# Performance work log

Hardware: AMD Instinct MI355X
Metric: run time of the kernel (lower is better)

The kernel has to match this reference:

```python
import jax, jax.numpy as jnp
import numpy as np

NEG = -1.0e9
LN_EPS = 1e-5

B, S, M = 16, 1024, 256
H, L = 8, 2
DK = M // H  # 32


def setup_inputs() -> dict:
    key = jax.random.key(0)
    ks = jax.random.split(key, 10)
    adj = jax.random.randint(ks[0], (B, S, S), 0, 2).astype(jnp.int32)
    inputs = jax.random.normal(ks[1], (B, S, M), dtype=jnp.float32)
    score_mask = jax.random.randint(ks[2], (B, 1, S, S), 0, 2).astype(bool)
    # learned params: per layer H head projections Linear(M, DK), one attn Linear(2*DK, 1), LayerNorm(M)
    sc = 1.0 / np.sqrt(M)
    proj_w = jax.random.uniform(ks[3], (L, H, M, DK), jnp.float32, -sc, sc)
    proj_b = jax.random.uniform(ks[4], (L, H, DK), jnp.float32, -sc, sc)
    sa = 1.0 / np.sqrt(2 * DK)
    attn_w = jax.random.uniform(ks[5], (L, 2 * DK), jnp.float32, -sa, sa)
    attn_b = jax.random.uniform(ks[6], (L,), jnp.float32, -sa, sa)
    ln_g = jnp.ones((L, M), jnp.float32)
    ln_b = jnp.zeros((L, M), jnp.float32)
    return {"adj": adj, "inputs": inputs, "score_mask": score_mask, "type": 0,
            "proj_w": proj_w, "proj_b": proj_b, "attn_w": attn_w, "attn_b": attn_b,
            "ln_g": ln_g, "ln_b": ln_b}


def _layer(x, adj_l, smask, pw, pb, aw, ab, g, b):
    # x: [B,S,M]; per-head projection -> [B,H,S,DK]
    P = jnp.einsum('bsm,hmd->bhsd', x, pw) + pb[None, :, None, :]
    a1, a2 = aw[:DK], aw[DK:]
    # additive attention decomposed: score[b,h,i,j] = leaky_relu(a1.P_i + a2.P_j + ab)
    s1 = jnp.einsum('bhsd,d->bhs', P, a1)
    s2 = jnp.einsum('bhsd,d->bhs', P, a2)
    score = s1[..., :, None] + s2[..., None, :] + ab
    score = jnp.where(score >= 0, score, 0.2 * score)  # leaky_relu(0.2)
    score = jnp.where(smask, NEG, score)               # score_mask[:,0] broadcast over heads
    if adj_l is not None:
        score = jnp.where(adj_l[:, None] == 0, NEG, score)
    attn = jax.nn.softmax(score, axis=-1)
    out = jnp.einsum('bhij,bhjd->bhid', attn, P)       # [B,H,S,DK]
    concat = out.transpose(0, 2, 1, 3).reshape(x.shape[0], x.shape[1], -1)
    r = x + concat
    mu = jnp.mean(r, axis=-1, keepdims=True)
    var = jnp.mean((r - mu) ** 2, axis=-1, keepdims=True)
    return (r - mu) * jax.lax.rsqrt(var + LN_EPS) * g + b


def reference(adj, inputs, score_mask, type, proj_w, proj_b, attn_w, attn_b, ln_g, ln_b):
    # eval mode: DropBlock and both dropouts are identity
    semantic = (type == 1)
    smask = score_mask[:, 0][:, None]  # [B,1,S,S]
    x = inputs
    for l in range(L):
        adj_l = None if (semantic and l > 0) else adj
        x = _layer(x, adj_l, smask, proj_w[l], proj_b[l], attn_w[l], attn_b[l], ln_g[l], ln_b[l])
    return x
```

## Files before the change

### kernel.cpp

```cpp
#include <hip/hip_runtime.h>
#include <hip/hip_bf16.h>
#include <hip/hip_fp16.h>
#include <math.h>

#define NB 16
#define NS 1024
#define NM 256
#define NH 8
#define NDK 32
#define NL 2

typedef __attribute__((ext_vector_type(4))) float f32x4;
typedef __attribute__((ext_vector_type(8))) short bf16x8;
typedef __attribute__((ext_vector_type(4))) short bf16x4u;
typedef __attribute__((ext_vector_type(8))) _Float16 f16x8;
typedef __attribute__((ext_vector_type(2))) _Float16 f16x2;

#if __has_builtin(__builtin_amdgcn_exp2f)
#define EXP2F(x) __builtin_amdgcn_exp2f(x)
#else
#define EXP2F(x) exp2f(x)
#endif

__device__ __forceinline__ unsigned short f2h(float f) {
  _Float16 h = (_Float16)f;
  return __builtin_bit_cast(unsigned short, h);
}

__device__ __forceinline__ unsigned int wword(unsigned int pw, unsigned int nw,
                                              f16x2 e1p2, f16x2 e1n2,
                                              unsigned int mk) {
  f16x2 hp = __builtin_bit_cast(f16x2, pw);
  f16x2 hn = __builtin_bit_cast(f16x2, nw);
  f16x2 w = __builtin_elementwise_max(hp * e1p2, hn * e1n2);
  return __builtin_bit_cast(unsigned int, w) & mk;
}

__global__ __launch_bounds__(256) void packbits_kernel(
    const int* __restrict__ src, unsigned int* __restrict__ dst, int inv,
    unsigned int* __restrict__ orc)
{
  int wid = blockIdx.x * 4 + (threadIdx.x >> 6);
  int lane = threadIdx.x & 63;
  size_t eb = (size_t)wid * 2048;
  const int4* a4 = (const int4*)(src + eb);
  int lg = lane >> 3;
  int sh = (lane & 7) * 4;
  unsigned int xo = inv ? 15u : 0u;
#pragma unroll
  for (int k = 0; k < 8; ++k) {
    int4 v = a4[k * 64 + lane];
    unsigned int nc = ((v.x != 0) ? 1u : 0u) | ((v.y != 0) ? 2u : 0u) |
                      ((v.z != 0) ? 4u : 0u) | ((v.w != 0) ? 8u : 0u);
    nc ^= xo;
    unsigned int vc = nc << sh;
    vc |= __shfl_xor(vc, 1, 64);
    vc |= __shfl_xor(vc, 2, 64);
    vc |= __shfl_xor(vc, 4, 64);
    if ((lane & 7) == 0) {
      size_t wi = (size_t)wid * 64 + k * 8 + lg;
      dst[wi] = vc;
      if (orc) orc[wi] |= vc;
    }
  }
}

__global__ __launch_bounds__(256) void wprep_kernel(
    const float* __restrict__ pw, unsigned short* __restrict__ Wt)
{
  __shared__ float lw[256][36];
  int lh = blockIdx.x;
  int t = threadIdx.x;
  const float* src = pw + (size_t)lh * NM * NDK;
#pragma unroll
  for (int q = 0; q < 8; ++q) {
    int e0 = q * 1024 + t * 4;
    int m = e0 >> 5, dc = e0 & 31;
    f32x4 v = *(const f32x4*)(src + e0);
    *(f32x4*)&lw[m][dc] = v;
  }
  __syncthreads();
  unsigned short* out = Wt + (size_t)lh * NDK * NM;
#pragma unroll
  for (int q = 0; q < 4; ++q) {
    int idx = q * 2048 + t * 8;
    int d = idx >> 8, m = idx & 255;
    unsigned short ov[8];
#pragma unroll
    for (int j = 0; j < 8; ++j) ov[j] = f2h(lw[m + j][d]);
    *(uint4*)(out + (size_t)d * NM + m) = *(uint4*)ov;
  }
}

__global__ __launch_bounds__(256) void proj_kernel(
    const float* __restrict__ x,
    const unsigned short* __restrict__ Wt,
    const float* __restrict__ pb,
    const float* __restrict__ aw,
    const float* __restrict__ abp,
    unsigned short* __restrict__ Pt,
    float* __restrict__ s1o,
    unsigned short* __restrict__ s2po,
    unsigned short* __restrict__ s2no)
{
  __shared__ unsigned short As[64][40];
  __shared__ unsigned short Bs[64][40];

  const float LOG2E = 1.4426950408889634f;
  int ct = blockIdx.x;
  int rt = blockIdx.y;
  int t = threadIdx.x;
  int w = t >> 6, lane = t & 63;
  int il = lane & 15, g4 = lane >> 4;
  int wi = w >> 1, wc = w & 1;

  f32x4 acc[2][2] = {};

  int arow = t >> 2, akoff = (t & 3) * 8;
  int brow = t >> 2, bkoff = (t & 3) * 8;

  for (int k0 = 0; k0 < NM; k0 += 32) {
    const float* xp = x + (size_t)(rt * 64 + arow) * NM + k0 + akoff;
    f32x4 v0 = *(const f32x4*)xp;
    f32x4 v1 = *(const f32x4*)(xp + 4);
    unsigned short av[8];
    av[0] = f2h(v0[0]); av[1] = f2h(v0[1]); av[2] = f2h(v0[2]); av[3] = f2h(v0[3]);
    av[4] = f2h(v1[0]); av[5] = f2h(v1[1]); av[6] = f2h(v1[2]); av[7] = f2h(v1[3]);
    *(uint4*)&As[arow][akoff] = *(uint4*)av;
    uint4 bv = *(const uint4*)(Wt + (size_t)(ct * 64 + brow) * NM + k0 + bkoff);
    *(uint4*)&Bs[brow][bkoff] = bv;
    __syncthreads();

    f16x8 af0 = *(f16x8*)&As[wi * 32 + il][g4 * 8];
    f16x8 af1 = *(f16x8*)&As[wi * 32 + 16 + il][g4 * 8];
    f16x8 bf0 = *(f16x8*)&Bs[wc * 32 + il][g4 * 8];
    f16x8 bf1 = *(f16x8*)&Bs[wc * 32 + 16 + il][g4 * 8];
    acc[0][0] = __builtin_amdgcn_mfma_f32_16x16x32_f16(af0, bf0, acc[0][0], 0, 0, 0);
    acc[0][1] = __builtin_amdgcn_mfma_f32_16x16x32_f16(af0, bf1, acc[0][1], 0, 0, 0);
    acc[1][0] = __builtin_amdgcn_mfma_f32_16x16x32_f16(af1, bf0, acc[1][0], 0, 0, 0);
    acc[1][1] = __builtin_amdgcn_mfma_f32_16x16x32_f16(af1, bf1, acc[1][1], 0, 0, 0);
    __syncthreads();
  }

  int head = ct * 2 + wc;
  float a1v[2] = {aw[il], aw[16 + il]};
  float a2v[2] = {aw[32 + il], aw[48 + il]};
  float ab = abp[0];

#pragma unroll
  for (int ih = 0; ih < 2; ++ih) {
    float s1p[4] = {0.f, 0.f, 0.f, 0.f};
    float s2p[4] = {0.f, 0.f, 0.f, 0.f};
    int r0 = rt * 64 + wi * 32 + ih * 16 + g4 * 4;
    int bb = r0 >> 10, ss = r0 & 1023;
#pragma unroll
    for (int dh = 0; dh < 2; ++dh) {
      int colhd = ct * 64 + wc * 32 + dh * 16 + il;
      int dd = colhd & 31;
      float bias = pb[colhd];
      f32x4 c = acc[ih][dh];
      unsigned short ov[4];
#pragma unroll
      for (int e = 0; e < 4; ++e) {
        float Pv = c[e] + bias;
        ov[e] = f2h(Pv);
        s1p[e] += Pv * a1v[dh];
        s2p[e] += Pv * a2v[dh];
      }
      size_t idx = ((size_t)(bb * NH + head) * NDK + dd) * NS + ss;
      *(bf16x4u*)(Pt + idx) = *(bf16x4u*)ov;
    }
#pragma unroll
    for (int e = 0; e < 4; ++e) {
#pragma unroll
      for (int off = 1; off <= 8; off <<= 1) {
        s1p[e] += __shfl_xor(s1p[e], off, 64);
        s2p[e] += __shfl_xor(s2p[e], off, 64);
      }
    }
    if (il == 0) {
      size_t sb = (size_t)(bb * NH + head) * NS + ss;
#pragma unroll
      for (int e = 0; e < 4; ++e) {
        s1o[sb + e] = s1p[e] * LOG2E;
        float s2L = (s2p[e] + ab) * LOG2E;
        s2L = fminf(fmaxf(s2L, -7.5f), 7.5f);
        s2po[sb + e] = f2h(EXP2F(s2L));
        s2no[sb + e] = f2h(EXP2F(0.2f * s2L));
      }
    }
  }
}

__global__ __launch_bounds__(512) void attn_kernel(
    const unsigned short* __restrict__ Pt,
    const float* __restrict__ s1a,
    const unsigned short* __restrict__ s2pa,
    const unsigned short* __restrict__ s2na,
    const unsigned int* __restrict__ pkc,
    const unsigned int* __restrict__ pks,
    const int* __restrict__ typep,
    int layer,
    float* __restrict__ co)
{
  __shared__ __align__(16) unsigned short ptl[32 * 512];
  __shared__ __align__(16) unsigned short e2pl[1024];
  __shared__ __align__(16) unsigned short e2nl[1024];
  __shared__ uint4 mtab[256];

  int orig = blockIdx.x;
  int lb = (orig & 7) * 64 + (orig >> 3);
  int iq = lb & 3, bh = lb >> 2;
  int b = bh >> 3, h = bh & 7;

  int t = threadIdx.x, w = t >> 6, lane = t & 63;
  int il = lane & 15, g4 = lane >> 4;
  int xorv = (il & 7) << 4;

  if (t < 256) {
    unsigned int m = t;
    uint4 e;
    e.x = ((m & 1u)   ? 0u : 0xFFFFu) | ((m & 2u)   ? 0u : 0xFFFF0000u);
    e.y = ((m & 4u)   ? 0u : 0xFFFFu) | ((m & 8u)   ? 0u : 0xFFFF0000u);
    e.z = ((m & 16u)  ? 0u : 0xFFFFu) | ((m & 32u)  ? 0u : 0xFFFF0000u);
    e.w = ((m & 64u)  ? 0u : 0xFFFFu) | ((m & 128u) ? 0u : 0xFFFF0000u);
    mtab[t] = e;
  }

  const unsigned char* pkb =
      (const unsigned char*)((typep[0] == 1 && layer > 0) ? pks : pkc);
  const unsigned short* ptg = Pt + (size_t)bh * NDK * NS;

  f16x8 ones;
#pragma unroll
  for (int e = 0; e < 8; ++e) ones[e] = (_Float16)1.0f;

  int rbase = iq * 256 + w * 32;
  f16x2 e1p2[2], e1n2[2];
  const unsigned char* mrow[2];
#pragma unroll
  for (int g = 0; g < 2; ++g) {
    float s1L = s1a[(size_t)bh * NS + rbase + g * 16 + il];
    s1L = fminf(fmaxf(s1L, -7.5f), 7.5f);
    _Float16 hp = (_Float16)EXP2F(s1L);
    _Float16 hn = (_Float16)EXP2F(0.2f * s1L);
    e1p2[g][0] = hp; e1p2[g][1] = hp;
    e1n2[g][0] = hn; e1n2[g][1] = hn;
    mrow[g] = pkb + (((size_t)(b * NS + rbase + g * 16 + il) * NS) >> 3);
  }

  f32x4 acc[2][2] = {};
  f32x4 accd[2] = {};

  for (int jh = 0; jh < 2; ++jh) {
    __syncthreads();
    {
      const char* srcb = (const char*)ptg;
#pragma unroll
      for (int q = 0; q < 4; ++q) {
        int pos = q * 8192 + t * 16;
        int r = pos >> 10;
        int incol = pos & 1023;
        uint4 v = *(const uint4*)(srcb + r * 2048 + jh * 1024 + incol);
        *(uint4*)((char*)ptl + r * 1024 + (incol ^ ((r & 7) << 4))) = v;
      }
      if (jh == 0) {
        if (t < 128)
          ((uint4*)e2pl)[t] = *(const uint4*)(s2pa + (size_t)bh * NS + t * 8);
        else if (t < 256)
          ((uint4*)e2nl)[t - 128] =
              *(const uint4*)(s2na + (size_t)bh * NS + (t - 128) * 8);
      }
    }
    __syncthreads();

    for (int jg = 0; jg < 512; jg += 128) {
      uint4 mk0 = *(const uint4*)(mrow[0] + ((jh * 512 + jg) >> 3));
      uint4 mk1 = *(const uint4*)(mrow[1] + ((jh * 512 + jg) >> 3));
#pragma unroll
      for (int s = 0; s < 4; ++s) {
        unsigned int mb0 = ((&mk0.x)[s] >> (g4 * 8)) & 0xFFu;
        unsigned int mb1 = ((&mk1.x)[s] >> (g4 * 8)) & 0xFFu;
        uint4 am0 = mtab[mb0];
        uint4 am1 = mtab[mb1];
        int jl = jg + s * 32 + g4 * 8;
        int coff = (jl * 2) ^ xorv;
        const char* prow = (const char*)ptl + il * 1024;
        f16x8 b0 = *(const f16x8*)(prow + coff);
        f16x8 b1 = *(const f16x8*)(prow + 16 * 1024 + coff);
        int jfull = jh * 512 + jl;
        uint4 p4 = *(const uint4*)&e2pl[jfull];
        uint4 n4 = *(const uint4*)&e2nl[jfull];
        uint4 w0, w1;
        w0.x = wword(p4.x, n4.x, e1p2[0], e1n2[0], am0.x);
        w0.y = wword(p4.y, n4.y, e1p2[0], e1n2[0], am0.y);
        w0.z = wword(p4.z, n4.z, e1p2[0], e1n2[0], am0.z);
        w0.w = wword(p4.w, n4.w, e1p2[0], e1n2[0], am0.w);
        w1.x = wword(p4.x, n4.x, e1p2[1], e1n2[1], am1.x);
        w1.y = wword(p4.y, n4.y, e1p2[1], e1n2[1], am1.y);
        w1.z = wword(p4.z, n4.z, e1p2[1], e1n2[1], am1.z);
        w1.w = wword(p4.w, n4.w, e1p2[1], e1n2[1], am1.w);
        f16x8 af0 = __builtin_bit_cast(f16x8, w0);
        f16x8 af1 = __builtin_bit_cast(f16x8, w1);
        acc[0][0] = __builtin_amdgcn_mfma_f32_16x16x32_f16(af0, b0, acc[0][0], 0, 0, 0);
        acc[0][1] = __builtin_amdgcn_mfma_f32_16x16x32_f16(af0, b1, acc[0][1], 0, 0, 0);
        accd[0]   = __builtin_amdgcn_mfma_f32_16x16x32_f16(af0, ones, accd[0], 0, 0, 0);
        acc[1][0] = __builtin_amdgcn_mfma_f32_16x16x32_f16(af1, b0, acc[1][0], 0, 0, 0);
        acc[1][1] = __builtin_amdgcn_mfma_f32_16x16x32_f16(af1, b1, acc[1][1], 0, 0, 0);
        accd[1]   = __builtin_amdgcn_mfma_f32_16x16x32_f16(af1, ones, accd[1], 0, 0, 0);
      }
    }
  }

#pragma unroll
  for (int g = 0; g < 2; ++g) {
    f32x4 rd;
#pragma unroll
    for (int e = 0; e < 4; ++e) rd[e] = __builtin_amdgcn_rcpf(accd[g][e]);
    float* cob = co + (size_t)(b * NS + rbase + g * 16 + g4 * 4) * NM + h * 32 + il;
#pragma unroll
    for (int e = 0; e < 4; ++e) {
      cob[(size_t)e * NM] = acc[g][0][e] * rd[e];
      cob[(size_t)e * NM + 16] = acc[g][1][e] * rd[e];
    }
  }
}

__global__ __launch_bounds__(256) void ln_kernel(
    const float* __restrict__ xin, const float* __restrict__ co,
    const float* __restrict__ lng, const float* __restrict__ lnb,
    float* __restrict__ xout)
{
  int row = blockIdx.x * 4 + (threadIdx.x >> 6);
  int lane = threadIdx.x & 63;
  size_t base = (size_t)row * NM + lane * 4;
  f32x4 cv = *(const f32x4*)(co + base);
  f32x4 xv = *(const f32x4*)(xin + base);
  f32x4 r;
#pragma unroll
  for (int e = 0; e < 4; ++e) r[e] = cv[e] + xv[e];
  float sm = r[0] + r[1] + r[2] + r[3];
  float sq = r[0] * r[0] + r[1] * r[1] + r[2] * r[2] + r[3] * r[3];
#pragma unroll
  for (int off = 32; off >= 1; off >>= 1) {
    sm += __shfl_xor(sm, off, 64);
    sq += __shfl_xor(sq, off, 64);
  }
  float mu = sm * (1.f / 256.f);
  float var = sq * (1.f / 256.f) - mu * mu;
  float inv = rsqrtf(var + 1e-5f);
  f32x4 gv = *(const f32x4*)(lng + lane * 4);
  f32x4 bv = *(const f32x4*)(lnb + lane * 4);
  f32x4 o;
#pragma unroll
  for (int e = 0; e < 4; ++e) o[e] = (r[e] - mu) * inv * gv[e] + bv[e];
  *(f32x4*)(xout + base) = o;
}

extern "C" void kernel_launch(void* const* d_in, const int* in_sizes, int n_in,
                              void* d_out, int out_size, void* d_ws, size_t ws_size,
                              hipStream_t stream)
{
  const int* adj = (const int*)d_in[0];
  const float* inputs = (const float*)d_in[1];
  const int* smask = (const int*)d_in[2];
  const int* typep = (const int*)d_in[3];
  const float* proj_w = (const float*)d_in[4];
  const float* proj_b = (const float*)d_in[5];
  const float* attn_w = (const float*)d_in[6];
  const float* attn_b = (const float*)d_in[7];
  const float* ln_g = (const float*)d_in[8];
  const float* ln_b = (const float*)d_in[9];
  float* out = (float*)d_out;

  char* ws = (char*)d_ws;
  unsigned int* pkc = (unsigned int*)(ws);
  unsigned int* pks = (unsigned int*)(ws + (2u << 20));
  unsigned short* Pt = (unsigned short*)(ws + (4u << 20));
  float* s1 = (float*)(ws + (12u << 20));
  unsigned short* s2p = (unsigned short*)(ws + (12u << 20) + (1u << 19));
  unsigned short* s2n = (unsigned short*)(ws + (13u << 20));
  float* x1 = (float*)(ws + (14u << 20));
  unsigned short* Wt = (unsigned short*)(ws + (30u << 20));
  float* co = out;

  packbits_kernel<<<2048, 256, 0, stream>>>(adj, pkc, 1, nullptr);
  packbits_kernel<<<2048, 256, 0, stream>>>(smask, pks, 0, pkc);
  wprep_kernel<<<16, 256, 0, stream>>>(proj_w, Wt);

  for (int l = 0; l < NL; ++l) {
    const float* xin = (l == 0) ? inputs : x1;
    float* xout = (l == NL - 1) ? out : x1;
    proj_kernel<<<dim3(4, 256), 256, 0, stream>>>(
        xin, Wt + (size_t)l * NH * NDK * NM, proj_b + (size_t)l * NH * NDK,
        attn_w + l * 64, attn_b + l, Pt, s1, s2p, s2n);
    attn_kernel<<<512, 512, 0, stream>>>(
        Pt, s1, s2p, s2n, pkc, pks, typep, l, co);
    ln_kernel<<<4096, 256, 0, stream>>>(xin, co, ln_g + l * NM, ln_b + l * NM, xout);
  }
}
```

Before: 128.0 us.

## Fuse mask packing with layer-0 projection and store attention output as fp16

Both mask-packing launches and the first-layer projection now run as one combined prelude kernel. The read-modify-write OR of the score mask into the adjacency bitmap is removed, so the attention kernel loads both bitmaps and ORs them on the fly. The attention output is written as fp16 to a workspace buffer instead of fp32, which halves that traffic, and the layernorm kernel reads it back in fp16. The trade-offs are extra mask loads in the attention inner loop and lower precision on the attention output before the residual add.

```diff
diff --git a/kernel.cpp b/kernel.cpp
--- a/kernel.cpp
+++ b/kernel.cpp
@@ -11,7 +11,6 @@
 #define NL 2
 
 typedef __attribute__((ext_vector_type(4))) float f32x4;
-typedef __attribute__((ext_vector_type(8))) short bf16x8;
 typedef __attribute__((ext_vector_type(4))) short bf16x4u;
 typedef __attribute__((ext_vector_type(8))) _Float16 f16x8;
 typedef __attribute__((ext_vector_type(2))) _Float16 f16x2;
@@ -25,6 +24,9 @@
 __device__ __forceinline__ unsigned short f2h(float f) {
   _Float16 h = (_Float16)f;
   return __builtin_bit_cast(unsigned short, h);
+}
+__device__ __forceinline__ float h2f(unsigned short u) {
+  return (float)__builtin_bit_cast(_Float16, u);
 }
 
 __device__ __forceinline__ unsigned int wword(unsigned int pw, unsigned int nw,
@@ -36,35 +38,6 @@
   return __builtin_bit_cast(unsigned int, w) & mk;
 }
 
-__global__ __launch_bounds__(256) void packbits_kernel(
-    const int* __restrict__ src, unsigned int* __restrict__ dst, int inv,
-    unsigned int* __restrict__ orc)
-{
-  int wid = blockIdx.x * 4 + (threadIdx.x >> 6);
-  int lane = threadIdx.x & 63;
-  size_t eb = (size_t)wid * 2048;
-  const int4* a4 = (const int4*)(src + eb);
-  int lg = lane >> 3;
-  int sh = (lane & 7) * 4;
-  unsigned int xo = inv ? 15u : 0u;
-#pragma unroll
-  for (int k = 0; k < 8; ++k) {
-    int4 v = a4[k * 64 + lane];
-    unsigned int nc = ((v.x != 0) ? 1u : 0u) | ((v.y != 0) ? 2u : 0u) |
-                      ((v.z != 0) ? 4u : 0u) | ((v.w != 0) ? 8u : 0u);
-    nc ^= xo;
-    unsigned int vc = nc << sh;
-    vc |= __shfl_xor(vc, 1, 64);
-    vc |= __shfl_xor(vc, 2, 64);
-    vc |= __shfl_xor(vc, 4, 64);
-    if ((lane & 7) == 0) {
-      size_t wi = (size_t)wid * 64 + k * 8 + lg;
-      dst[wi] = vc;
-      if (orc) orc[wi] |= vc;
-    }
-  }
-}
-
 __global__ __launch_bounds__(256) void wprep_kernel(
     const float* __restrict__ pw, unsigned short* __restrict__ Wt)
 {
@@ -92,32 +65,22 @@
   }
 }
 
-__global__ __launch_bounds__(256) void proj_kernel(
-    const float* __restrict__ x,
-    const unsigned short* __restrict__ Wt,
-    const float* __restrict__ pb,
-    const float* __restrict__ aw,
+__device__ __forceinline__ void proj_body(
+    int ct, int rt, int t,
+    const float* __restrict__ x, const unsigned short* __restrict__ Wt,
+    const float* __restrict__ pb, const float* __restrict__ aw,
     const float* __restrict__ abp,
-    unsigned short* __restrict__ Pt,
-    float* __restrict__ s1o,
-    unsigned short* __restrict__ s2po,
-    unsigned short* __restrict__ s2no)
-{
-  __shared__ unsigned short As[64][40];
-  __shared__ unsigned short Bs[64][40];
-
+    unsigned short* __restrict__ Pt, float* __restrict__ s1o,
+    unsigned short* __restrict__ s2po, unsigned short* __restrict__ s2no,
+    unsigned short (*As)[40], unsigned short (*Bs)[40])
+{
   const float LOG2E = 1.4426950408889634f;
-  int ct = blockIdx.x;
-  int rt = blockIdx.y;
-  int t = threadIdx.x;
   int w = t >> 6, lane = t & 63;
   int il = lane & 15, g4 = lane >> 4;
   int wi = w >> 1, wc = w & 1;
 
   f32x4 acc[2][2] = {};
-
   int arow = t >> 2, akoff = (t & 3) * 8;
-  int brow = t >> 2, bkoff = (t & 3) * 8;
 
   for (int k0 = 0; k0 < NM; k0 += 32) {
     const float* xp = x + (size_t)(rt * 64 + arow) * NM + k0 + akoff;
@@ -127,8 +90,8 @@
     av[0] = f2h(v0[0]); av[1] = f2h(v0[1]); av[2] = f2h(v0[2]); av[3] = f2h(v0[3]);
     av[4] = f2h(v1[0]); av[5] = f2h(v1[1]); av[6] = f2h(v1[2]); av[7] = f2h(v1[3]);
     *(uint4*)&As[arow][akoff] = *(uint4*)av;
-    uint4 bv = *(const uint4*)(Wt + (size_t)(ct * 64 + brow) * NM + k0 + bkoff);
-    *(uint4*)&Bs[brow][bkoff] = bv;
+    uint4 bv = *(const uint4*)(Wt + (size_t)(ct * 64 + arow) * NM + k0 + akoff);
+    *(uint4*)&Bs[arow][akoff] = bv;
     __syncthreads();
 
     f16x8 af0 = *(f16x8*)&As[wi * 32 + il][g4 * 8];
@@ -192,16 +155,72 @@
   }
 }
 
+__global__ __launch_bounds__(256) void prelude_kernel(
+    const int* __restrict__ adj, const int* __restrict__ smask,
+    unsigned int* __restrict__ pka, unsigned int* __restrict__ pks,
+    const float* __restrict__ x, const unsigned short* __restrict__ Wt0,
+    const float* __restrict__ pb0, const float* __restrict__ aw0,
+    const float* __restrict__ ab0,
+    unsigned short* __restrict__ Pt, float* __restrict__ s1o,
+    unsigned short* __restrict__ s2po, unsigned short* __restrict__ s2no)
+{
+  __shared__ unsigned short As[64][40];
+  __shared__ unsigned short Bs[64][40];
+
+  int bid = blockIdx.x;
+  int t = threadIdx.x;
+  if (bid < 4096) {
+    const int* src = (bid < 2048) ? adj : smask;
+    unsigned int* dst = (bid < 2048) ? pka : pks;
+    unsigned int xo = (bid < 2048) ? 15u : 0u;
+    int wid = (bid & 2047) * 4 + (t >> 6);
+    int lane = t & 63;
+    size_t eb = (size_t)wid * 2048;
+    const int4* a4 = (const int4*)(src + eb);
+    int lg = lane >> 3;
+    int sh = (lane & 7) * 4;
+#pragma unroll
+    for (int k = 0; k < 8; ++k) {
+      int4 v = a4[k * 64 + lane];
+      unsigned int nc = ((v.x != 0) ? 1u : 0u) | ((v.y != 0) ? 2u : 0u) |
+                        ((v.z != 0) ? 4u : 0u) | ((v.w != 0) ? 8u : 0u);
+      nc ^= xo;
+      unsigned int vc = nc << sh;
+      vc |= __shfl_xor(vc, 1, 64);
+      vc |= __shfl_xor(vc, 2, 64);
+      vc |= __shfl_xor(vc, 4, 64);
+      if ((lane & 7) == 0) dst[(size_t)wid * 64 + k * 8 + lg] = vc;
+    }
+  } else {
+    int pb2 = bid - 4096;
+    proj_body(pb2 & 3, pb2 >> 2, t, x, Wt0, pb0, aw0, ab0,
+              Pt, s1o, s2po, s2no, As, Bs);
+  }
+}
+
+__global__ __launch_bounds__(256) void proj_kernel(
+    const float* __restrict__ x, const unsigned short* __restrict__ Wt,
+    const float* __restrict__ pb, const float* __restrict__ aw,
+    const float* __restrict__ abp,
+    unsigned short* __restrict__ Pt, float* __restrict__ s1o,
+    unsigned short* __restrict__ s2po, unsigned short* __restrict__ s2no)
+{
+  __shared__ unsigned short As[64][40];
+  __shared__ unsigned short Bs[64][40];
+  proj_body(blockIdx.x, blockIdx.y, threadIdx.x, x, Wt, pb, aw, abp,
+            Pt, s1o, s2po, s2no, As, Bs);
+}
+
 __global__ __launch_bounds__(512) void attn_kernel(
     const unsigned short* __restrict__ Pt,
     const float* __restrict__ s1a,
     const unsigned short* __restrict__ s2pa,
     const unsigned short* __restrict__ s2na,
-    const unsigned int* __restrict__ pkc,
+    const unsigned int* __restrict__ pka,
     const unsigned int* __restrict__ pks,
     const int* __restrict__ typep,
     int layer,
-    float* __restrict__ co)
+    unsigned short* __restrict__ co)
 {
   __shared__ __align__(16) unsigned short ptl[32 * 512];
   __shared__ __align__(16) unsigned short e2pl[1024];
@@ -227,8 +246,9 @@
     mtab[t] = e;
   }
 
-  const unsigned char* pkb =
-      (const unsigned char*)((typep[0] == 1 && layer > 0) ? pks : pkc);
+  bool comb = !(typep[0] == 1 && layer > 0);
+  const unsigned char* pa = (const unsigned char*)(comb ? pka : pks);
+  const unsigned char* ps = (const unsigned char*)pks;
   const unsigned short* ptg = Pt + (size_t)bh * NDK * NS;
 
   f16x8 ones;
@@ -237,7 +257,7 @@
 
   int rbase = iq * 256 + w * 32;
   f16x2 e1p2[2], e1n2[2];
-  const unsigned char* mrow[2];
+  size_t mbyte[2];
 #pragma unroll
   for (int g = 0; g < 2; ++g) {
     float s1L = s1a[(size_t)bh * NS + rbase + g * 16 + il];
@@ -246,7 +266,7 @@
     _Float16 hn = (_Float16)EXP2F(0.2f * s1L);
     e1p2[g][0] = hp; e1p2[g][1] = hp;
     e1n2[g][0] = hn; e1n2[g][1] = hn;
-    mrow[g] = pkb + (((size_t)(b * NS + rbase + g * 16 + il) * NS) >> 3);
+    mbyte[g] = ((size_t)(b * NS + rbase + g * 16 + il) * NS) >> 3;
   }
 
   f32x4 acc[2][2] = {};
@@ -275,8 +295,16 @@
     __syncthreads();
 
     for (int jg = 0; jg < 512; jg += 128) {
-      uint4 mk0 = *(const uint4*)(mrow[0] + ((jh * 512 + jg) >> 3));
-      uint4 mk1 = *(const uint4*)(mrow[1] + ((jh * 512 + jg) >> 3));
+      size_t off = (size_t)((jh * 512 + jg) >> 3);
+      uint4 ka0 = *(const uint4*)(pa + mbyte[0] + off);
+      uint4 ks0 = *(const uint4*)(ps + mbyte[0] + off);
+      uint4 ka1 = *(const uint4*)(pa + mbyte[1] + off);
+      uint4 ks1 = *(const uint4*)(ps + mbyte[1] + off);
+      uint4 mk0, mk1;
+      mk0.x = ka0.x | ks0.x; mk0.y = ka0.y | ks0.y;
+      mk0.z = ka0.z | ks0.z; mk0.w = ka0.w | ks0.w;
+      mk1.x = ka1.x | ks1.x; mk1.y = ka1.y | ks1.y;
+      mk1.z = ka1.z | ks1.z; mk1.w = ka1.w | ks1.w;
 #pragma unroll
       for (int s = 0; s < 4; ++s) {
         unsigned int mb0 = ((&mk0.x)[s] >> (g4 * 8)) & 0xFFu;
@@ -317,28 +345,31 @@
     f32x4 rd;
 #pragma unroll
     for (int e = 0; e < 4; ++e) rd[e] = __builtin_amdgcn_rcpf(accd[g][e]);
-    float* cob = co + (size_t)(b * NS + rbase + g * 16 + g4 * 4) * NM + h * 32 + il;
+    unsigned short* cob =
+        co + (size_t)(b * NS + rbase + g * 16 + g4 * 4) * NM + h * 32 + il;
 #pragma unroll
     for (int e = 0; e < 4; ++e) {
-      cob[(size_t)e * NM] = acc[g][0][e] * rd[e];
-      cob[(size_t)e * NM + 16] = acc[g][1][e] * rd[e];
+      cob[(size_t)e * NM] = f2h(acc[g][0][e] * rd[e]);
+      cob[(size_t)e * NM + 16] = f2h(acc[g][1][e] * rd[e]);
     }
   }
 }
 
 __global__ __launch_bounds__(256) void ln_kernel(
-    const float* __restrict__ xin, const float* __restrict__ co,
+    const float* __restrict__ xin, const unsigned short* __restrict__ co,
     const float* __restrict__ lng, const float* __restrict__ lnb,
     float* __restrict__ xout)
 {
   int row = blockIdx.x * 4 + (threadIdx.x >> 6);
   int lane = threadIdx.x & 63;
   size_t base = (size_t)row * NM + lane * 4;
-  f32x4 cv = *(const f32x4*)(co + base);
+  ushort4 cv = *(const ushort4*)(co + base);
   f32x4 xv = *(const f32x4*)(xin + base);
   f32x4 r;
-#pragma unroll
-  for (int e = 0; e < 4; ++e) r[e] = cv[e] + xv[e];
+  r[0] = xv[0] + h2f(cv.x);
+  r[1] = xv[1] + h2f(cv.y);
+  r[2] = xv[2] + h2f(cv.z);
+  r[3] = xv[3] + h2f(cv.w);
   float sm = r[0] + r[1] + r[2] + r[3];
   float sq = r[0] * r[0] + r[1] * r[1] + r[2] * r[2] + r[3] * r[3];
 #pragma unroll
@@ -374,7 +405,7 @@
   float* out = (float*)d_out;
 
   char* ws = (char*)d_ws;
-  unsigned int* pkc = (unsigned int*)(ws);
+  unsigned int* pka = (unsigned int*)(ws);
   unsigned int* pks = (unsigned int*)(ws + (2u << 20));
   unsigned short* Pt = (unsigned short*)(ws + (4u << 20));
   float* s1 = (float*)(ws + (12u << 20));
@@ -382,20 +413,19 @@
   unsigned short* s2n = (unsigned short*)(ws + (13u << 20));
   float* x1 = (float*)(ws + (14u << 20));
   unsigned short* Wt = (unsigned short*)(ws + (30u << 20));
-  float* co = out;
-
-  packbits_kernel<<<2048, 256, 0, stream>>>(adj, pkc, 1, nullptr);
-  packbits_kernel<<<2048, 256, 0, stream>>>(smask, pks, 0, pkc);
+  unsigned short* co = (unsigned short*)(ws + (31u << 20));
+
   wprep_kernel<<<16, 256, 0, stream>>>(proj_w, Wt);
-
-  for (int l = 0; l < NL; ++l) {
-    const float* xin = (l == 0) ? inputs : x1;
-    float* xout = (l == NL - 1) ? out : x1;
-    proj_kernel<<<dim3(4, 256), 256, 0, stream>>>(
-        xin, Wt + (size_t)l * NH * NDK * NM, proj_b + (size_t)l * NH * NDK,
-        attn_w + l * 64, attn_b + l, Pt, s1, s2p, s2n);
-    attn_kernel<<<512, 512, 0, stream>>>(
-        Pt, s1, s2p, s2n, pkc, pks, typep, l, co);
-    ln_kernel<<<4096, 256, 0, stream>>>(xin, co, ln_g + l * NM, ln_b + l * NM, xout);
-  }
-}
+  prelude_kernel<<<5120, 256, 0, stream>>>(
+      adj, smask, pka, pks, inputs, Wt, proj_b, attn_w, attn_b,
+      Pt, s1, s2p, s2n);
+  attn_kernel<<<512, 512, 0, stream>>>(
+      Pt, s1, s2p, s2n, pka, pks, typep, 0, co);
+  ln_kernel<<<4096, 256, 0, stream>>>(inputs, co, ln_g, ln_b, x1);
+  proj_kernel<<<dim3(4, 256), 256, 0, stream>>>(
+      x1, Wt + (size_t)NH * NDK * NM, proj_b + (size_t)NH * NDK,
+      attn_w + 64, attn_b + 1, Pt, s1, s2p, s2n);
+  attn_kernel<<<512, 512, 0, stream>>>(
+      Pt, s1, s2p, s2n, pka, pks, typep, 1, co);
+  ln_kernel<<<4096, 256, 0, stream>>>(x1, co, ln_g + NM, ln_b + NM, out);
+}
```

Measured after the change: 120.2 us (median of 2 runs). -6.1%, faster.
